# Optimization experiments

Hardware: AMD Instinct MI355X
Metric: run time of the kernel (lower is better)

The kernel has to match this reference:

```python
import jax, jax.numpy as jnp
import numpy as np

B, ENC_T, ENC_D = 16, 600, 512
H = 512          # hidden_size == attn_dim (Attention built with attn_dim=hidden_size)
A = 512
VOCAB = 8000
MAX_LEN = 64
SOS = 1


def setup_inputs() -> dict:
    key = jax.random.key(0)
    ks = jax.random.split(key, 16)
    n = jax.random.normal
    s = 0.04  # param init scale
    return {
        "encoder_outputs": n(ks[0], (B, ENC_T, ENC_D), dtype=jnp.float32),
        # embedding table
        "emb": n(ks[1], (VOCAB, H)) * 0.05,
        # GRU (1 layer, input = hidden + enc_dim), PyTorch layout [3H, in]/[3H, H]
        "w_ih": n(ks[2], (3 * H, H + ENC_D)) * s,
        "w_hh": n(ks[3], (3 * H, H)) * s,
        "b_ih": n(ks[4], (3 * H,)) * s,
        "b_hh": n(ks[5], (3 * H,)) * s,
        # location attention: Conv1d(1 -> A, k=3, pad=1)
        "conv_w": n(ks[6], (A, 1, 3)) * 0.1,
        "conv_b": n(ks[7], (A,)) * 0.1,
        "attn_W": n(ks[8], (A, H)) * s,      # W: dec_dim -> attn_dim, no bias
        "attn_V": n(ks[9], (A, ENC_D)) * s,  # V: enc_dim -> attn_dim, no bias
        "attn_fc_w": n(ks[10], (1, A)) * s,  # fc: attn_dim -> 1, with bias
        "attn_fc_b": n(ks[11], (1,)) * s,
        "attn_b": n(ks[12], (A,)) * s,       # extra learned bias b
        # output projection: (hidden + enc_dim) -> vocab
        "fc_w": n(ks[13], (VOCAB, H + ENC_D)) * s,
        "fc_b": n(ks[14], (VOCAB,)) * s,
    }


def reference(encoder_outputs, emb, w_ih, w_hh, b_ih, b_hh,
              conv_w, conv_b, attn_W, attn_V, attn_fc_w, attn_fc_b, attn_b,
              fc_w, fc_b):
    dt = encoder_outputs.dtype
    b, t, ed = encoder_outputs.shape
    h_dim = emb.shape[1]

    # V(values) is time-invariant across decode steps: precompute once. [B, T, A]
    Vv = jnp.einsum('btd,ad->bta', encoder_outputs, attn_V)

    tok0 = jnp.full((b,), SOS, dtype=jnp.int32)
    h0 = jnp.zeros((b, h_dim), dt)          # GRU hidden (None -> zeros)
    ctx0 = jnp.zeros((b, ed), dt)           # initial context
    aw0 = jnp.zeros((b, t), dt)             # initial attention weights

    def step(carry, _):
        tok, h, ctx, aw = carry
        # embed + concat with previous context  [B, H+E]
        x = jnp.concatenate([emb[tok], ctx], axis=-1)
        # GRU cell (PyTorch gate order r, z, n)
        gx = x @ w_ih.T + b_ih
        gh = h @ w_hh.T + b_hh
        xr, xz, xn = jnp.split(gx, 3, axis=-1)
        hr, hz, hn = jnp.split(gh, 3, axis=-1)
        r = jax.nn.sigmoid(xr + hr)
        z = jax.nn.sigmoid(xz + hz)
        ncand = jnp.tanh(xn + r * hn)
        h_new = (1.0 - z) * ncand + z * h
        # location feature: Conv1d over last attention weights. [B, A, T] -> [B, T, A]
        conv = jax.lax.conv_general_dilated(
            aw[:, None, :], conv_w, window_strides=(1,), padding=[(1, 1)],
            dimension_numbers=('NCH', 'OIH', 'NCH')) + conv_b[None, :, None]
        conv = jnp.transpose(conv, (0, 2, 1))
        # score = fc(tanh(W(q) + V(values) + conv + b))  [B, T]
        wq = h_new @ attn_W.T                      # [B, A]
        e = jnp.tanh(wq[:, None, :] + Vv + conv + attn_b)
        score = jnp.einsum('bta,a->bt', e, attn_fc_w[0]) + attn_fc_b[0]
        aw_new = jax.nn.softmax(score, axis=-1)
        # context = attn_weight @ values  [B, E]
        ctx_new = jnp.einsum('bt,btd->bd', aw_new, encoder_outputs)
        # output projection + log_softmax
        out = jnp.concatenate([h_new, ctx_new], axis=-1)
        logits = out @ fc_w.T + fc_b
        logp = jax.nn.log_softmax(logits, axis=-1)
        tok_new = jnp.argmax(logp, axis=-1).astype(jnp.int32)  # greedy symbol
        return (tok_new, h_new, ctx_new, aw_new), logp

    _, logps = jax.lax.scan(step, (tok0, h0, ctx0, aw0), None, length=MAX_LEN)
    # [T_dec, B, V] -> [B, T_dec, V], matching stacked decoder_outputs
    return jnp.transpose(logps, (1, 0, 2))
```

## Files before the change

kernel.cpp:

```cpp
#include <hip/hip_runtime.h>
#include <math.h>

#define NG 256
#define NT 512
#define XSS 516
#define NLOGW 250

__device__ __forceinline__ void gbar(int* cnt, int epoch, int g, int tid) {
    __syncthreads();
    if (tid == 0) {
        int* c0 = cnt + ((g & 15) << 5);
        int* c1 = cnt + 512;
        int* go = cnt + 576;
        int r = __hip_atomic_fetch_add(c0, 1, __ATOMIC_RELEASE,
                                       __HIP_MEMORY_SCOPE_AGENT);
        if (r == (epoch << 4) - 1) {
            int r2 = __hip_atomic_fetch_add(c1, 1, __ATOMIC_RELAXED,
                                            __HIP_MEMORY_SCOPE_AGENT);
            if (r2 == (epoch << 4) - 1)
                __hip_atomic_store(go, epoch, __ATOMIC_RELAXED,
                                   __HIP_MEMORY_SCOPE_AGENT);
        }
        int it = 0;
        while (__hip_atomic_load(go, __ATOMIC_RELAXED,
                                 __HIP_MEMORY_SCOPE_AGENT) < epoch) {
            if (++it > 2) __builtin_amdgcn_s_sleep(16);
        }
        (void)__hip_atomic_load(go, __ATOMIC_ACQUIRE,
                                __HIP_MEMORY_SCOPE_AGENT);
    }
    __syncthreads();
}

__global__ __launch_bounds__(256) void k_vv(const float* __restrict__ enc,
                                            const float* __restrict__ attn_V,
                                            float* __restrict__ Vv) {
    int wg = blockIdx.x;
    int b = wg / 40, t0 = (wg % 40) * 15;
    int tid = threadIdx.x;
    __shared__ __align__(16) float encL[15][512];
    for (int i = tid; i < 15 * 512; i += 256) {
        int tl = i >> 9, d = i & 511;
        encL[tl][d] = enc[((size_t)(b * 600) + (t0 + tl)) * 512 + d];
    }
    __syncthreads();
    for (int half = 0; half < 2; ++half) {
        int a = tid + half * 256;
        const float4* wrow = reinterpret_cast<const float4*>(attn_V + (size_t)a * 512);
        float acc[15];
#pragma unroll
        for (int tl = 0; tl < 15; ++tl) acc[tl] = 0.f;
        for (int k = 0; k < 128; ++k) {
            float4 w = wrow[k];
#pragma unroll
            for (int tl = 0; tl < 15; ++tl) {
                float4 x = reinterpret_cast<const float4*>(&encL[tl][0])[k];
                acc[tl] += w.x * x.x + w.y * x.y + w.z * x.z + w.w * x.w;
            }
        }
        for (int tl = 0; tl < 15; ++tl)
            Vv[((size_t)(b * 600) + (t0 + tl)) * 512 + a] = acc[tl];
    }
}

__global__ __launch_bounds__(NT, 1) void mega(
    const float* __restrict__ enc, const float* __restrict__ emb,
    const float* __restrict__ w_ih, const float* __restrict__ w_hh,
    const float* __restrict__ b_ih, const float* __restrict__ b_hh,
    const float* __restrict__ conv_w, const float* __restrict__ conv_b,
    const float* __restrict__ attn_W, const float* __restrict__ attn_fc_w,
    const float* __restrict__ attn_fc_b, const float* __restrict__ attn_b,
    const float* __restrict__ fc_w, const float* __restrict__ fc_b,
    const float* __restrict__ Vv,
    float* hbuf, float* ctxg, float* awg, float* scoreg, float* wqg,
    float* part, float* logZ, int* cnt, float* dout)
{
    const int g = blockIdx.x;
    const int tid = threadIdx.x;
    int epoch = 0;

    __shared__ float xs[16 * XSS];
    __shared__ float aux[2600];


    for (int s = 0; s < 64; ++s) {
        const int p = s & 1;
        if (g < 128) {
            float* pg = aux;
            float* tokf = aux + 2048;
            if (s == 0) {
                if (tid < 16) tokf[tid] = 1.0f;
                __syncthreads();
            } else {
                const int wv = tid >> 6, lane = tid & 63;
                for (int b = wv; b < 16; b += 8) {
                    float M = -3.4e38f, S = 0.f, I = 0.f;
                    for (int q = 0; q < 4; ++q) {
                        int pw = lane + (q << 6);
                        if (pw < NLOGW) {
                            const float* r = part + ((size_t)pw * 16 + b) * 4;
                            float m = r[0], se = r[1], ii = r[2];
                            if (m > M)      { S = S * expf(M - m) + se; M = m; I = ii; }
                            else if (m == M){ S += se; if (ii < I) I = ii; }
                            else            { S += se * expf(m - M); }
                        }
                    }
                    for (int off = 32; off; off >>= 1) {
                        float m  = __shfl_xor(M, off, 64);
                        float se = __shfl_xor(S, off, 64);
                        float ii = __shfl_xor(I, off, 64);
                        if (m > M)      { S = S * expf(M - m) + se; M = m; I = ii; }
                        else if (m == M){ S += se; if (ii < I) I = ii; }
                        else            { S += se * expf(m - M); }
                    }
                    if (lane == 0) {
                        tokf[b] = I;
                        if (g == 0) logZ[(s - 1) * 16 + b] = M + logf(S);
                    }
                }
                __syncthreads();
            }
            const int b  = tid & 15;
            const int u  = tid >> 4;
            const int il = u & 3;
            const int pr = u >> 2;
            const int i  = (g << 2) + il;
            float ar = 0.f, az = 0.f, axn = 0.f, ahn = 0.f;
            for (int pass = 0; pass < 3; ++pass) {
                for (int idx = tid; idx < 8192; idx += NT) {
                    int bb = idx >> 9, k = idx & 511;
                    float v;
                    if (pass == 0)      v = emb[(size_t)((int)tokf[bb]) * 512 + k];
                    else if (pass == 1) v = ctxg[(bb << 9) + k];
                    else                v = hbuf[((p << 4) + bb) * 512 + k];
                    xs[bb * XSS + k] = v;
                }
                __syncthreads();
                const float* wbase = (pass == 2) ? w_hh : w_ih;
                const size_t rl = (pass == 2) ? 512 : 1024;
                const int ko = (pass == 1) ? 512 : 0;
                const float4* wr = (const float4*)(wbase + (size_t)i * rl + ko) + (pr << 4);
                const float4* wz = (const float4*)(wbase + (size_t)(512 + i) * rl + ko) + (pr << 4);
                const float4* wn = (const float4*)(wbase + (size_t)(1024 + i) * rl + ko) + (pr << 4);
                const float4* xv = (const float4*)(xs + b * XSS) + (pr << 4);
                float s0 = 0.f, s1 = 0.f, s2 = 0.f;
#pragma unroll 4
                for (int k = 0; k < 16; ++k) {
                    float4 x = xv[k];
                    float4 a = wr[k]; s0 += a.x*x.x + a.y*x.y + a.z*x.z + a.w*x.w;
                    float4 c = wz[k]; s1 += c.x*x.x + c.y*x.y + c.z*x.z + c.w*x.w;
                    float4 d = wn[k]; s2 += d.x*x.x + d.y*x.y + d.z*x.z + d.w*x.w;
                }
                ar += s0; az += s1;
                if (pass < 2) axn += s2; else ahn += s2;
                if (pass < 2) __syncthreads();
            }
            {
                int base = (((b << 2) + il) << 3) + pr;
                pg[base] = ar; pg[512 + base] = az;
                pg[1024 + base] = axn; pg[1536 + base] = ahn;
            }
            __syncthreads();
            if (tid < 64) {
                int bb = tid & 15, ill = tid >> 4;
                int ii = (g << 2) + ill;
                float sr = 0.f, sz2 = 0.f, sxn = 0.f, shn = 0.f;
                int bs = ((bb << 2) + ill) << 3;
                for (int q = 0; q < 8; ++q) {
                    sr  += pg[bs + q];        sz2 += pg[512 + bs + q];
                    sxn += pg[1024 + bs + q]; shn += pg[1536 + bs + q];
                }
                sr  += b_ih[ii] + b_hh[ii];
                sz2 += b_ih[512 + ii] + b_hh[512 + ii];
                sxn += b_ih[1024 + ii];
                shn += b_hh[1024 + ii];
                float r = 1.f / (1.f + expf(-sr));
                float z = 1.f / (1.f + expf(-sz2));
                float n = tanhf(sxn + r * shn);
                float hp = xs[bb * XSS + ii];
                hbuf[(((p ^ 1) << 4) + bb) * 512 + ii] = (1.f - z) * n + z * hp;
            }
        }
        gbar(cnt, ++epoch, g, tid);

        {
            const int b = g & 15, ac = g >> 4;
            for (int idx = tid; idx < 512; idx += NT)
                xs[idx] = hbuf[(((p ^ 1) << 4) + b) * 512 + idx];
            __syncthreads();
            const int al = tid >> 4, ln = tid & 15;
            const int a = (ac << 5) + al;
            const float4* wr = (const float4*)(attn_W + (size_t)a * 512) + (ln << 3);
            const float4* hv = (const float4*)xs + (ln << 3);
            float acc = 0.f;
#pragma unroll
            for (int k = 0; k < 8; ++k) {
                float4 w = wr[k], x = hv[k];
                acc += w.x*x.x + w.y*x.y + w.z*x.z + w.w*x.w;
            }
            for (int off = 8; off; off >>= 1) acc += __shfl_xor(acc, off, 64);
            if (ln == 0) wqg[(b << 9) + a] = acc;
        }
        gbar(cnt, ++epoch, g, tid);

        {
            const int b = g & 15, tc = g >> 4;
            const int t0 = tc * 38;
            float* wqL  = xs;
            float* cw0  = xs + 512;
            float* cw1  = xs + 1024;
            float* cw2  = xs + 1536;
            float* cbab = xs + 2048;
            float* fcwL = xs + 2560;
            for (int a = tid; a < 512; a += NT) {
                wqL[a]  = wqg[(b << 9) + a];
                cw0[a]  = conv_w[a * 3];
                cw1[a]  = conv_w[a * 3 + 1];
                cw2[a]  = conv_w[a * 3 + 2];
                cbab[a] = conv_b[a] + attn_b[a];
                fcwL[a] = attn_fc_w[a];
            }
            __syncthreads();
            const float fcb = attn_fc_b[0];
            const int wv = tid >> 6, lane = tid & 63;
            for (int tl = wv; tl < 38; tl += 8) {
                const int t = t0 + tl;
                if (t < 600) {
                    const float awm = (t > 0)   ? awg[b * 600 + t - 1] : 0.f;
                    const float aw0 = awg[b * 600 + t];
                    const float awp = (t < 599) ? awg[b * 600 + t + 1] : 0.f;
                    const float* vv = Vv + ((size_t)b * 600 + t) * 512;
                    float acc = 0.f;
#pragma unroll
                    for (int q = 0; q < 8; ++q) {
                        const int a = lane + (q << 6);
                        float uu = wqL[a] + vv[a] + cbab[a]
                                 + cw0[a] * awm + cw1[a] * aw0 + cw2[a] * awp;
                        acc += tanhf(uu) * fcwL[a];
                    }
                    for (int off = 32; off; off >>= 1) acc += __shfl_xor(acc, off, 64);
                    if (lane == 0) scoreg[b * 600 + t] = acc + fcb;
                }
            }
        }
        gbar(cnt, ++epoch, g, tid);

        {
            const int b = g & 15, ec = g >> 4;
            float* pb    = xs;
            float* wredM = aux + 2064;
            float* wredS = aux + 2080;
            float* red16 = aux;
            float lm = -3.4e38f;
            for (int t = tid; t < 600; t += NT) {
                float v = scoreg[b * 600 + t];
                pb[t] = v;
                lm = fmaxf(lm, v);
            }
            for (int off = 32; off; off >>= 1) lm = fmaxf(lm, __shfl_xor(lm, off, 64));
            if ((tid & 63) == 0) wredM[tid >> 6] = lm;
            __syncthreads();
            float M = wredM[0];
#pragma unroll
            for (int q = 1; q < 8; ++q) M = fmaxf(M, wredM[q]);
            float lsum = 0.f;
            for (int t = tid; t < 600; t += NT) {
                float e = expf(pb[t] - M);
                pb[t] = e;
                lsum += e;
            }
            for (int off = 32; off; off >>= 1) lsum += __shfl_xor(lsum, off, 64);
            if ((tid & 63) == 0) wredS[tid >> 6] = lsum;
            __syncthreads();
            float S = 0.f;
#pragma unroll
            for (int q = 0; q < 8; ++q) S += wredS[q];
            const float invS = 1.f / S;
            if (ec == 0)
                for (int t = tid; t < 600; t += NT) awg[b * 600 + t] = pb[t] * invS;
            const int tg = tid >> 5, l32 = tid & 31;
            const int e = (ec << 5) + l32;
            float acc = 0.f;
            for (int t = tg; t < 600; t += 16)
                acc += pb[t] * enc[((size_t)b * 600 + t) * 512 + e];
            red16[(tg << 5) + l32] = acc;
            __syncthreads();
            if (tg == 0) {
                float a2 = 0.f;
#pragma unroll
                for (int q = 0; q < 16; ++q) a2 += red16[(q << 5) + l32];
                ctxg[(b << 9) + e] = a2 * invS;
            }
        }
        gbar(cnt, ++epoch, g, tid);

        {
            float* accL = aux;
            float acc0 = 0.f, acc1 = 0.f;
            const int bb = tid & 15, jj = (tid >> 4) & 15;
            const int act = (tid < 256);
            const int v0 = (g << 5) + (jj << 1);
            for (int pass = 0; pass < 2; ++pass) {
                for (int idx = tid; idx < 8192; idx += NT) {
                    int b2 = idx >> 9, k = idx & 511;
                    xs[b2 * XSS + k] = pass ? ctxg[(b2 << 9) + k]
                                            : hbuf[(((p ^ 1) << 4) + b2) * 512 + k];
                }
                __syncthreads();
                if (g < NLOGW && act) {
                    const float4* w0 = (const float4*)(fc_w + (size_t)v0 * 1024 + (pass << 9));
                    const float4* w1 = (const float4*)(fc_w + (size_t)(v0 + 1) * 1024 + (pass << 9));
                    const float4* xv = (const float4*)(xs + bb * XSS);
#pragma unroll 4
                    for (int k = 0; k < 128; ++k) {
                        float4 x = xv[k];
                        float4 a = w0[k]; acc0 += a.x*x.x + a.y*x.y + a.z*x.z + a.w*x.w;
                        float4 c = w1[k]; acc1 += c.x*x.x + c.y*x.y + c.z*x.z + c.w*x.w;
                    }
                }
                __syncthreads();
            }
            if (g < NLOGW && act) {
                acc0 += fc_b[v0]; acc1 += fc_b[v0 + 1];
                float* o = dout + ((size_t)bb * 64 + s) * 8000;
                o[v0] = acc0; o[v0 + 1] = acc1;
                float bv, bi;
                if (acc0 >= acc1) { bv = acc0; bi = (float)v0; }
                else              { bv = acc1; bi = (float)(v0 + 1); }
                float se = expf(acc0 - bv) + expf(acc1 - bv);
                int rbase = (((bb << 4) + jj) << 2);
                accL[rbase] = bv; accL[rbase + 1] = bi; accL[rbase + 2] = se;
            }
            __syncthreads();
            if (g < NLOGW && tid < 16) {
                float M = -3.4e38f, I = 0.f, S = 0.f;
                for (int q = 0; q < 16; ++q) {
                    int rb = (((tid << 4) + q) << 2);
                    float m = accL[rb], ii = accL[rb + 1], se = accL[rb + 2];
                    if (m > M)      { S = S * expf(M - m) + se; M = m; I = ii; }
                    else if (m == M){ S += se; if (ii < I) I = ii; }
                    else            { S += se * expf(m - M); }
                }
                float* pr2 = part + ((size_t)g * 16 + tid) * 4;
                pr2[0] = M; pr2[1] = S; pr2[2] = I;
            }
        }
        gbar(cnt, ++epoch, g, tid);
    }

    if (g == 0) {
        const int wv = tid >> 6, lane = tid & 63;
        for (int b = wv; b < 16; b += 8) {
            float M = -3.4e38f, S = 0.f;
            for (int q = 0; q < 4; ++q) {
                int pw = lane + (q << 6);
                if (pw < NLOGW) {
                    const float* r = part + ((size_t)pw * 16 + b) * 4;
                    float m = r[0], se = r[1];
                    if (m > M)      { S = S * expf(M - m) + se; M = m; }
                    else if (m == M){ S += se; }
                    else            { S += se * expf(m - M); }
                }
            }
            for (int off = 32; off; off >>= 1) {
                float m  = __shfl_xor(M, off, 64);
                float se = __shfl_xor(S, off, 64);
                if (m > M)      { S = S * expf(M - m) + se; M = m; }
                else if (m == M){ S += se; }
                else            { S += se * expf(m - M); }
            }
            if (lane == 0) logZ[63 * 16 + b] = M + logf(S);
        }
    }
    gbar(cnt, ++epoch, g, tid);
    for (int r = g; r < 1024; r += NG) {
        float z = logZ[(r & 63) * 16 + (r >> 6)];
        float* o = dout + (size_t)r * 8000;
        for (int i = tid; i < 8000; i += NT) o[i] -= z;
    }
}

extern "C" void kernel_launch(void* const* d_in, const int* in_sizes, int n_in,
                              void* d_out, int out_size, void* d_ws, size_t ws_size,
                              hipStream_t stream) {
    const float* enc       = (const float*)d_in[0];
    const float* emb       = (const float*)d_in[1];
    const float* w_ih      = (const float*)d_in[2];
    const float* w_hh      = (const float*)d_in[3];
    const float* b_ih      = (const float*)d_in[4];
    const float* b_hh      = (const float*)d_in[5];
    const float* conv_w    = (const float*)d_in[6];
    const float* conv_b    = (const float*)d_in[7];
    const float* attn_W    = (const float*)d_in[8];
    const float* attn_V    = (const float*)d_in[9];
    const float* attn_fc_w = (const float*)d_in[10];
    const float* attn_fc_b = (const float*)d_in[11];
    const float* attn_b    = (const float*)d_in[12];
    const float* fc_w      = (const float*)d_in[13];
    const float* fc_b      = (const float*)d_in[14];

    float* ws    = (float*)d_ws;
    float* Vv    = ws;
    float* hbuf  = Vv + 4915200;
    float* ctx   = hbuf + 16384;
    float* aw    = ctx + 8192;
    float* score = aw + 9600;
    float* wq    = score + 9600;
    float* part  = wq + 8192;
    float* logZ  = part + 16384;
    int*   cnt   = (int*)(logZ + 1024);
    float* dout  = (float*)d_out;

    hipMemsetAsync(hbuf, 0, 34176 * sizeof(float), stream);
    hipMemsetAsync(cnt, 0, 1024 * sizeof(int), stream);

    k_vv<<<dim3(640), dim3(256), 0, stream>>>(enc, attn_V, Vv);

    void* args[] = {(void*)&enc, (void*)&emb, (void*)&w_ih, (void*)&w_hh,
                    (void*)&b_ih, (void*)&b_hh, (void*)&conv_w, (void*)&conv_b,
                    (void*)&attn_W, (void*)&attn_fc_w, (void*)&attn_fc_b,
                    (void*)&attn_b, (void*)&fc_w, (void*)&fc_b, (void*)&Vv,
                    (void*)&hbuf, (void*)&ctx, (void*)&aw, (void*)&score,
                    (void*)&wq, (void*)&part, (void*)&logZ, (void*)&cnt,
                    (void*)&dout};
    hipLaunchCooperativeKernel(reinterpret_cast<void*>(mega),
                               dim3(NG), dim3(NT), args, 0, stream);
}
```

Measured before the change: 7.263 ms.

## Replace grid-barrier release/acquire fences with relaxed atomic loads/stores on shared buffers

Drops the release ordering on the barrier counter increment and the trailing acquire load. Instead, every cross-workgroup buffer (hidden state, context, attention weights, scores, partial logits, logZ) is now read and written through relaxed agent-scope atomics, so the data bypasses non-coherent caches without full cache flush/invalidate fences at each of the many per-step barriers. The spin loop's sleep policy is also adjusted. Correctness now relies on relaxed atomics plus the workgroup barrier being enough for ordering, which the memory model does not strictly guarantee.

```diff
diff --git a/kernel.cpp b/kernel.cpp
--- a/kernel.cpp
+++ b/kernel.cpp
@@ -5,6 +5,13 @@
 #define NT 512
 #define XSS 516
 #define NLOGW 250
+
+__device__ __forceinline__ float ldc(const float* p) {
+    return __hip_atomic_load(p, __ATOMIC_RELAXED, __HIP_MEMORY_SCOPE_AGENT);
+}
+__device__ __forceinline__ void stc(float* p, float v) {
+    __hip_atomic_store(p, v, __ATOMIC_RELAXED, __HIP_MEMORY_SCOPE_AGENT);
+}
 
 __device__ __forceinline__ void gbar(int* cnt, int epoch, int g, int tid) {
     __syncthreads();
@@ -12,7 +19,7 @@
         int* c0 = cnt + ((g & 15) << 5);
         int* c1 = cnt + 512;
         int* go = cnt + 576;
-        int r = __hip_atomic_fetch_add(c0, 1, __ATOMIC_RELEASE,
+        int r = __hip_atomic_fetch_add(c0, 1, __ATOMIC_RELAXED,
                                        __HIP_MEMORY_SCOPE_AGENT);
         if (r == (epoch << 4) - 1) {
             int r2 = __hip_atomic_fetch_add(c1, 1, __ATOMIC_RELAXED,
@@ -24,10 +31,8 @@
         int it = 0;
         while (__hip_atomic_load(go, __ATOMIC_RELAXED,
                                  __HIP_MEMORY_SCOPE_AGENT) < epoch) {
-            if (++it > 2) __builtin_amdgcn_s_sleep(16);
-        }
-        (void)__hip_atomic_load(go, __ATOMIC_ACQUIRE,
-                                __HIP_MEMORY_SCOPE_AGENT);
+            if (++it > 4) __builtin_amdgcn_s_sleep(8);
+        }
     }
     __syncthreads();
 }
@@ -99,7 +104,7 @@
                         int pw = lane + (q << 6);
                         if (pw < NLOGW) {
                             const float* r = part + ((size_t)pw * 16 + b) * 4;
-                            float m = r[0], se = r[1], ii = r[2];
+                            float m = ldc(r), se = ldc(r + 1), ii = ldc(r + 2);
                             if (m > M)      { S = S * expf(M - m) + se; M = m; I = ii; }
                             else if (m == M){ S += se; if (ii < I) I = ii; }
                             else            { S += se * expf(m - M); }
@@ -115,7 +120,7 @@
                     }
                     if (lane == 0) {
                         tokf[b] = I;
-                        if (g == 0) logZ[(s - 1) * 16 + b] = M + logf(S);
+                        if (g == 0) stc(&logZ[(s - 1) * 16 + b], M + logf(S));
                     }
                 }
                 __syncthreads();
@@ -131,8 +136,8 @@
                     int bb = idx >> 9, k = idx & 511;
                     float v;
                     if (pass == 0)      v = emb[(size_t)((int)tokf[bb]) * 512 + k];
-                    else if (pass == 1) v = ctxg[(bb << 9) + k];
-                    else                v = hbuf[((p << 4) + bb) * 512 + k];
+                    else if (pass == 1) v = ldc(&ctxg[(bb << 9) + k]);
+                    else                v = ldc(&hbuf[((p << 4) + bb) * 512 + k]);
                     xs[bb * XSS + k] = v;
                 }
                 __syncthreads();
@@ -178,7 +183,7 @@
                 float z = 1.f / (1.f + expf(-sz2));
                 float n = tanhf(sxn + r * shn);
                 float hp = xs[bb * XSS + ii];
-                hbuf[(((p ^ 1) << 4) + bb) * 512 + ii] = (1.f - z) * n + z * hp;
+                stc(&hbuf[(((p ^ 1) << 4) + bb) * 512 + ii], (1.f - z) * n + z * hp);
             }
         }
         gbar(cnt, ++epoch, g, tid);
@@ -186,7 +191,7 @@
         {
             const int b = g & 15, ac = g >> 4;
             for (int idx = tid; idx < 512; idx += NT)
-                xs[idx] = hbuf[(((p ^ 1) << 4) + b) * 512 + idx];
+                xs[idx] = ldc(&hbuf[(((p ^ 1) << 4) + b) * 512 + idx]);
             __syncthreads();
             const int al = tid >> 4, ln = tid & 15;
             const int a = (ac << 5) + al;
@@ -199,7 +204,7 @@
                 acc += w.x*x.x + w.y*x.y + w.z*x.z + w.w*x.w;
             }
             for (int off = 8; off; off >>= 1) acc += __shfl_xor(acc, off, 64);
-            if (ln == 0) wqg[(b << 9) + a] = acc;
+            if (ln == 0) stc(&wqg[(b << 9) + a], acc);
         }
         gbar(cnt, ++epoch, g, tid);
 
@@ -213,7 +218,7 @@
             float* cbab = xs + 2048;
             float* fcwL = xs + 2560;
             for (int a = tid; a < 512; a += NT) {
-                wqL[a]  = wqg[(b << 9) + a];
+                wqL[a]  = ldc(&wqg[(b << 9) + a]);
                 cw0[a]  = conv_w[a * 3];
                 cw1[a]  = conv_w[a * 3 + 1];
                 cw2[a]  = conv_w[a * 3 + 2];
@@ -226,9 +231,9 @@
             for (int tl = wv; tl < 38; tl += 8) {
                 const int t = t0 + tl;
                 if (t < 600) {
-                    const float awm = (t > 0)   ? awg[b * 600 + t - 1] : 0.f;
-                    const float aw0 = awg[b * 600 + t];
-                    const float awp = (t < 599) ? awg[b * 600 + t + 1] : 0.f;
+                    const float awm = (t > 0)   ? ldc(&awg[b * 600 + t - 1]) : 0.f;
+                    const float aw0 = ldc(&awg[b * 600 + t]);
+                    const float awp = (t < 599) ? ldc(&awg[b * 600 + t + 1]) : 0.f;
                     const float* vv = Vv + ((size_t)b * 600 + t) * 512;
                     float acc = 0.f;
 #pragma unroll
@@ -239,7 +244,7 @@
                         acc += tanhf(uu) * fcwL[a];
                     }
                     for (int off = 32; off; off >>= 1) acc += __shfl_xor(acc, off, 64);
-                    if (lane == 0) scoreg[b * 600 + t] = acc + fcb;
+                    if (lane == 0) stc(&scoreg[b * 600 + t], acc + fcb);
                 }
             }
         }
@@ -253,7 +258,7 @@
             float* red16 = aux;
             float lm = -3.4e38f;
             for (int t = tid; t < 600; t += NT) {
-                float v = scoreg[b * 600 + t];
+                float v = ldc(&scoreg[b * 600 + t]);
                 pb[t] = v;
                 lm = fmaxf(lm, v);
             }
@@ -277,7 +282,7 @@
             for (int q = 0; q < 8; ++q) S += wredS[q];
             const float invS = 1.f / S;
             if (ec == 0)
-                for (int t = tid; t < 600; t += NT) awg[b * 600 + t] = pb[t] * invS;
+                for (int t = tid; t < 600; t += NT) stc(&awg[b * 600 + t], pb[t] * invS);
             const int tg = tid >> 5, l32 = tid & 31;
             const int e = (ec << 5) + l32;
             float acc = 0.f;
@@ -289,7 +294,7 @@
                 float a2 = 0.f;
 #pragma unroll
                 for (int q = 0; q < 16; ++q) a2 += red16[(q << 5) + l32];
-                ctxg[(b << 9) + e] = a2 * invS;
+                stc(&ctxg[(b << 9) + e], a2 * invS);
             }
         }
         gbar(cnt, ++epoch, g, tid);
@@ -303,8 +308,8 @@
             for (int pass = 0; pass < 2; ++pass) {
                 for (int idx = tid; idx < 8192; idx += NT) {
                     int b2 = idx >> 9, k = idx & 511;
-                    xs[b2 * XSS + k] = pass ? ctxg[(b2 << 9) + k]
-                                            : hbuf[(((p ^ 1) << 4) + b2) * 512 + k];
+                    xs[b2 * XSS + k] = pass ? ldc(&ctxg[(b2 << 9) + k])
+                                            : ldc(&hbuf[(((p ^ 1) << 4) + b2) * 512 + k]);
                 }
                 __syncthreads();
                 if (g < NLOGW && act) {
@@ -323,7 +328,8 @@
             if (g < NLOGW && act) {
                 acc0 += fc_b[v0]; acc1 += fc_b[v0 + 1];
                 float* o = dout + ((size_t)bb * 64 + s) * 8000;
-                o[v0] = acc0; o[v0 + 1] = acc1;
+                stc(o + v0, acc0);
+                stc(o + v0 + 1, acc1);
                 float bv, bi;
                 if (acc0 >= acc1) { bv = acc0; bi = (float)v0; }
                 else              { bv = acc1; bi = (float)(v0 + 1); }
@@ -342,7 +348,7 @@
                     else            { S += se * expf(m - M); }
                 }
                 float* pr2 = part + ((size_t)g * 16 + tid) * 4;
-                pr2[0] = M; pr2[1] = S; pr2[2] = I;
+                stc(pr2, M); stc(pr2 + 1, S); stc(pr2 + 2, I);
             }
         }
         gbar(cnt, ++epoch, g, tid);
@@ -356,7 +362,7 @@
                 int pw = lane + (q << 6);
                 if (pw < NLOGW) {
                     const float* r = part + ((size_t)pw * 16 + b) * 4;
-                    float m = r[0], se = r[1];
+                    float m = ldc(r), se = ldc(r + 1);
                     if (m > M)      { S = S * expf(M - m) + se; M = m; }
                     else if (m == M){ S += se; }
                     else            { S += se * expf(m - M); }
@@ -369,12 +375,12 @@
                 else if (m == M){ S += se; }
                 else            { S += se * expf(m - M); }
             }
-            if (lane == 0) logZ[63 * 16 + b] = M + logf(S);
+            if (lane == 0) stc(&logZ[63 * 16 + b], M + logf(S));
         }
     }
     gbar(cnt, ++epoch, g, tid);
     for (int r = g; r < 1024; r += NG) {
-        float z = logZ[(r & 63) * 16 + (r >> 6)];
+        float z = ldc(&logZ[(r & 63) * 16 + (r >> 6)]);
         float* o = dout + (size_t)r * 8000;
         for (int i = tid; i < 8000; i += NT) o[i] -= z;
     }
```

New measurement: 6.548 ms. 1.11x faster.
